# Kernel tuning notes

Measured on AMD Instinct MI355X. Metric: run time of the kernel, lower is better.

The kernel has to match this reference:

```python
import jax, jax.numpy as jnp
import numpy as np

B, C, H, W, K = 16, 512, 64, 64, 64  # K = external-attention latent dim (self.k = 64)


def setup_inputs() -> dict:
    key = jax.random.key(0)
    ks = jax.random.split(key, 5)
    x = jax.random.normal(ks[0], (B, C, H, W), dtype=jnp.float32)
    # conv1: Conv2d(c, c, 1) with bias; init normal(0, sqrt(2/(1*1*out_channels)))
    conv1_w = jax.random.normal(ks[1], (C, C), dtype=jnp.float32) * np.float32(np.sqrt(2.0 / C))
    conv1_b = jnp.zeros((C,), dtype=jnp.float32)
    # linear_0: Conv1d(c, k, 1, bias=False); init normal(0, sqrt(2/out_channels))
    lin0_w = jax.random.normal(ks[2], (K, C), dtype=jnp.float32) * np.float32(np.sqrt(2.0 / K))
    # linear_1: Conv1d(k, c, 1, bias=False)
    lin1_w = jax.random.normal(ks[3], (C, K), dtype=jnp.float32) * np.float32(np.sqrt(2.0 / C))
    # conv2: Conv2d(c, c, 1, bias=False)
    conv2_w = jax.random.normal(ks[4], (C, C), dtype=jnp.float32) * np.float32(np.sqrt(2.0 / C))
    return {"x": x, "conv1_w": conv1_w, "conv1_b": conv1_b,
            "lin0_w": lin0_w, "lin1_w": lin1_w, "conv2_w": conv2_w}


def reference(x, conv1_w, conv1_b, lin0_w, lin1_w, conv2_w):
    b, c, h, w = x.shape
    n = h * w
    idn = x
    # conv1: 1x1 conv == per-pixel GEMM
    y = jnp.einsum('oc,bchw->bohw', conv1_w, x) + conv1_b[None, :, None, None]
    y = y.reshape(b, c, n)
    # external attention: linear_0 -> softmax over tokens -> L1 renorm over latent dim
    attn = jnp.einsum('kc,bcn->bkn', lin0_w, y)          # (b, K, n)
    attn = jax.nn.softmax(attn, axis=-1)
    attn = attn / (1e-9 + attn.sum(axis=1, keepdims=True))
    y = jnp.einsum('ck,bkn->bcn', lin1_w, attn)          # (b, c, n)
    # rank: view(-1, c) row-major (as torch .view does), per-row topk threshold,
    # scale below-threshold by 0.75 and the rest by 1.25; output is detached
    # (torch.tensor(pred, requires_grad=False)) -> stop_gradient
    top_k = c // 2
    flat = y.reshape(-1, c)                               # (b*n, c) row-major chunks
    thr = jax.lax.top_k(flat, top_k)[0][:, -1:]           # k-th largest per row
    scaled = jnp.where(flat < thr, 0.75 * flat, 1.25 * flat)
    yr = jax.lax.stop_gradient(scaled).reshape(b, c, h, w)
    # conv2: 1x1 conv no bias + ReLU, residual add, final ReLU
    out = jax.nn.relu(jnp.einsum('oc,bchw->bohw', conv2_w, yr))
    return jax.nn.relu(out + idn)
```

## Files before the change

kernel.cpp:

```cpp
#include <hip/hip_runtime.h>
#include <stdint.h>

typedef unsigned short u16;
typedef unsigned int u32;
using short8 = __attribute__((ext_vector_type(8))) short;
using f32x4  = __attribute__((ext_vector_type(4))) float;

#define BDIM 16
#define CDIM 512
#define KLAT 64
#define NTOK 4096

__device__ __forceinline__ u16 f2bf(float x) {
  union { float f; u32 u; } a; a.f = x;
  u32 r = a.u + 0x7FFFu + ((a.u >> 16) & 1u);
  return (u16)(r >> 16);
}
__device__ __forceinline__ u32 pack2(float a, float b) {
  return (u32)f2bf(a) | ((u32)f2bf(b) << 16);
}

__global__ __launch_bounds__(256) void k_setup(
    const float* __restrict__ conv1_w, const float* __restrict__ conv1_b,
    const float* __restrict__ lin0_w,  const float* __restrict__ lin1_w,
    const float* __restrict__ conv2_w,
    u16* __restrict__ w0bf, float* __restrict__ b0,
    u16* __restrict__ lin1bf, u16* __restrict__ cwbf)
{
  const int bid = blockIdx.x;
  const int t = threadIdx.x;
  if (bid < 128) {
    const int kb = bid & 15, cb = bid >> 4;
    const int lane = t & 63;
    int k = kb * 4 + (t >> 6);
    k = __builtin_amdgcn_readfirstlane(k);
    const int c = cb * 64 + lane;
    float acc = 0.f;
    const float* l0 = lin0_w + (size_t)k * CDIM;
    const float* cw = conv1_w + c;
#pragma unroll 4
    for (int o = 0; o < CDIM; ++o)
      acc = fmaf(l0[o], cw[(size_t)o * CDIM], acc);
    w0bf[k * CDIM + c] = f2bf(acc);
  } else if (bid == 128) {
    if (t < KLAT) {
      float acc = 0.f;
      for (int c = 0; c < CDIM; ++c) acc = fmaf(lin0_w[t * CDIM + c], conv1_b[c], acc);
      b0[t] = acc;
    }
  } else if (bid < 193) {
    const int b2 = bid - 129;
    const float4* src = (const float4*)conv2_w;
#pragma unroll
    for (int i = 0; i < 4; ++i) {
      int idx = (b2 * 256 + t) + i * 16384;
      float4 v = src[idx];
      uint2 o;
      o.x = pack2(v.x, v.y);
      o.y = pack2(v.z, v.w);
      *(uint2*)(cwbf + (size_t)idx * 4) = o;
    }
  } else {
    const int b2 = bid - 193;
#pragma unroll
    for (int i = 0; i < 4; ++i) {
      int g = b2 * 1024 + i * 256 + t;
      float4 v0 = *(const float4*)(lin1_w + (size_t)g * 8);
      float4 v1 = *(const float4*)(lin1_w + (size_t)g * 8 + 4);
      uint4 o;
      o.x = pack2(v0.x, v0.y); o.y = pack2(v0.z, v0.w);
      o.z = pack2(v1.x, v1.y); o.w = pack2(v1.z, v1.w);
      *(uint4*)(lin1bf + (size_t)g * 8) = o;
    }
  }
}

__global__ __launch_bounds__(256) void k_xpose(
    const float* __restrict__ x, u16* __restrict__ xbt)
{
  __shared__ float tile[32 * 512];
  const int n0 = blockIdx.x * 512, c0 = blockIdx.y * 32, b = blockIdx.z;
  const int t = threadIdx.x;
#pragma unroll
  for (int i = 0; i < 16; ++i) {
    int f4 = t + i * 256;
    int row = f4 >> 7, col4 = f4 & 127;
    float4 v = *(const float4*)(x + ((size_t)(b * CDIM + c0 + row)) * NTOK + n0 + col4 * 4);
    int phys4 = (col4 + row + (row >> 3)) & 127;
    *(float4*)&tile[row * 512 + phys4 * 4] = v;
  }
  __syncthreads();
#pragma unroll
  for (int i = 0; i < 8; ++i) {
    int nr = (t >> 2) + i * 64;
    int cs = (t & 3) * 8;
    float w[8];
#pragma unroll
    for (int j = 0; j < 8; ++j) {
      int row = cs + j;
      int phys4 = ((nr >> 2) + row + (row >> 3)) & 127;
      w[j] = tile[row * 512 + phys4 * 4 + (nr & 3)];
    }
    uint4 o;
    o.x = pack2(w[0], w[1]); o.y = pack2(w[2], w[3]);
    o.z = pack2(w[4], w[5]); o.w = pack2(w[6], w[7]);
    *(uint4*)(xbt + ((size_t)(b * NTOK + n0 + nr)) * CDIM + c0 + cs) = o;
  }
}

__global__ __launch_bounds__(256) void k_logits(
    const u16* __restrict__ w0bf, const u16* __restrict__ xbt,
    const float* __restrict__ b0, float* __restrict__ logits)
{
  __shared__ u16 As[64 * 72];
  __shared__ u16 Bs[128 * 72];
  const int nb = blockIdx.x, b = blockIdx.y;
  const int t = threadIdx.x;
  const int wv = t >> 6, lane = t & 63;
  const int quad = lane >> 4, l15 = lane & 15;
  f32x4 acc[4][2];
#pragma unroll
  for (int mi = 0; mi < 4; ++mi)
#pragma unroll
    for (int ni = 0; ni < 2; ++ni) acc[mi][ni] = (f32x4){0.f, 0.f, 0.f, 0.f};

  for (int kc = 0; kc < 8; ++kc) {
#pragma unroll
    for (int i = 0; i < 2; ++i) {
      int ch = t + i * 256;
      int row = ch >> 3, col = (ch & 7) * 8;
      uint4 a = *(const uint4*)(w0bf + (size_t)row * CDIM + kc * 64 + col);
      *(uint4*)&As[row * 72 + col] = a;
    }
#pragma unroll
    for (int i = 0; i < 4; ++i) {
      int ch = t + i * 256;
      int row = ch >> 3, col = (ch & 7) * 8;
      uint4 bb = *(const uint4*)(xbt + ((size_t)(b * NTOK + nb * 128 + row)) * CDIM + kc * 64 + col);
      *(uint4*)&Bs[row * 72 + col] = bb;
    }
    __syncthreads();
#pragma unroll
    for (int kk = 0; kk < 2; ++kk) {
      short8 af[4], bf_[2];
#pragma unroll
      for (int mi = 0; mi < 4; ++mi)
        af[mi] = *(short8*)&As[(mi * 16 + l15) * 72 + kk * 32 + quad * 8];
#pragma unroll
      for (int ni = 0; ni < 2; ++ni)
        bf_[ni] = *(short8*)&Bs[(wv * 32 + ni * 16 + l15) * 72 + kk * 32 + quad * 8];
#pragma unroll
      for (int mi = 0; mi < 4; ++mi)
#pragma unroll
        for (int ni = 0; ni < 2; ++ni)
          acc[mi][ni] = __builtin_amdgcn_mfma_f32_16x16x32_bf16(
              af[mi], bf_[ni], acc[mi][ni], 0, 0, 0);
    }
    __syncthreads();
  }
#pragma unroll
  for (int mi = 0; mi < 4; ++mi) {
#pragma unroll
    for (int ni = 0; ni < 2; ++ni) {
#pragma unroll
      for (int r = 0; r < 4; ++r) {
        int row = mi * 16 + quad * 4 + r;
        int col = nb * 128 + wv * 32 + ni * 16 + l15;
        logits[((size_t)(b * KLAT + row)) * NTOK + col] = acc[mi][ni][r] + b0[row];
      }
    }
  }
}

__global__ __launch_bounds__(256) void k_softmax(float* __restrict__ attn)
{
  __shared__ float red[4], red2[4];
  const int t = threadIdx.x;
  float* p = attn + (size_t)blockIdx.x * NTOK;
  float4 v[4];
#pragma unroll
  for (int i = 0; i < 4; ++i) v[i] = ((float4*)p)[t + i * 256];
  float m = v[0].x;
#pragma unroll
  for (int i = 0; i < 4; ++i)
    m = fmaxf(m, fmaxf(fmaxf(v[i].x, v[i].y), fmaxf(v[i].z, v[i].w)));
#pragma unroll
  for (int o = 1; o < 64; o <<= 1) m = fmaxf(m, __shfl_xor(m, o));
  const int wv = t >> 6, lane = t & 63;
  if (lane == 0) red[wv] = m;
  __syncthreads();
  m = fmaxf(fmaxf(red[0], red[1]), fmaxf(red[2], red[3]));
  float s = 0.f;
#pragma unroll
  for (int i = 0; i < 4; ++i) {
    v[i].x = __expf(v[i].x - m); s += v[i].x;
    v[i].y = __expf(v[i].y - m); s += v[i].y;
    v[i].z = __expf(v[i].z - m); s += v[i].z;
    v[i].w = __expf(v[i].w - m); s += v[i].w;
  }
#pragma unroll
  for (int o = 1; o < 64; o <<= 1) s += __shfl_xor(s, o);
  if (lane == 0) red2[wv] = s;
  __syncthreads();
  s = red2[0] + red2[1] + red2[2] + red2[3];
  const float inv = 1.f / s;
#pragma unroll
  for (int i = 0; i < 4; ++i) {
    v[i].x *= inv; v[i].y *= inv; v[i].z *= inv; v[i].w *= inv;
    ((float4*)p)[t + i * 256] = v[i];
  }
}

__global__ __launch_bounds__(256) void k_attnT(
    const float* __restrict__ attn, u16* __restrict__ attnT)
{
  __shared__ float tile[64 * 256];
  __shared__ float inv_[256];
  const int n0 = blockIdx.x * 256, b = blockIdx.y;
  const int t = threadIdx.x;
#pragma unroll
  for (int i = 0; i < 16; ++i) {
    int f4 = t + i * 256;
    int row = f4 >> 6, col4 = f4 & 63;
    float4 v = *(const float4*)(attn + ((size_t)(b * KLAT + row)) * NTOK + n0 + col4 * 4);
    int phys4 = (col4 + row + (row >> 3)) & 63;
    *(float4*)&tile[row * 256 + phys4 * 4] = v;
  }
  __syncthreads();
  {
    int n4 = t >> 2, sub = t & 3;
    float s = 0.f;
#pragma unroll
    for (int k = 0; k < 64; ++k) {
      int phys4 = (n4 + k + (k >> 3)) & 63;
      s += tile[k * 256 + phys4 * 4 + sub];
    }
    inv_[t] = 1.f / (1e-9f + s);
  }
  __syncthreads();
#pragma unroll
  for (int i = 0; i < 8; ++i) {
    int nr = (t >> 3) + i * 32;
    int cs = (t & 7) * 8;
    float sc = inv_[nr];
    float w[8];
#pragma unroll
    for (int j = 0; j < 8; ++j) {
      int row = cs + j;
      int phys4 = ((nr >> 2) + row + (row >> 3)) & 63;
      w[j] = tile[row * 256 + phys4 * 4 + (nr & 3)] * sc;
    }
    uint4 o;
    o.x = pack2(w[0], w[1]); o.y = pack2(w[2], w[3]);
    o.z = pack2(w[4], w[5]); o.w = pack2(w[6], w[7]);
    *(uint4*)(attnT + ((size_t)(b * NTOK + n0 + nr)) * KLAT + cs) = o;
  }
}

__global__ __launch_bounds__(256) void k_lin1mm(
    const u16* __restrict__ lin1bf, const u16* __restrict__ attnT,
    float* __restrict__ y2)
{
  __shared__ u16 As[128 * 72];
  __shared__ u16 Bs[128 * 72];
  const int nb = blockIdx.x, mb = blockIdx.y, b = blockIdx.z;
  const int t = threadIdx.x;
  const int wv = t >> 6, lane = t & 63;
  const int wm = wv >> 1, wn = wv & 1;
  const int quad = lane >> 4, l15 = lane & 15;
  f32x4 acc[4][4];
#pragma unroll
  for (int mi = 0; mi < 4; ++mi)
#pragma unroll
    for (int ni = 0; ni < 4; ++ni) acc[mi][ni] = (f32x4){0.f, 0.f, 0.f, 0.f};

#pragma unroll
  for (int i = 0; i < 4; ++i) {
    int ch = t + i * 256;
    int row = ch >> 3, col = (ch & 7) * 8;
    uint4 a = *(const uint4*)(lin1bf + ((size_t)(mb * 128 + row)) * KLAT + col);
    *(uint4*)&As[row * 72 + col] = a;
    uint4 bb = *(const uint4*)(attnT + ((size_t)(b * NTOK + nb * 128 + row)) * KLAT + col);
    *(uint4*)&Bs[row * 72 + col] = bb;
  }
  __syncthreads();
#pragma unroll
  for (int kk = 0; kk < 2; ++kk) {
    short8 af[4], bf_[4];
#pragma unroll
    for (int mi = 0; mi < 4; ++mi)
      af[mi] = *(short8*)&As[(wm * 64 + mi * 16 + l15) * 72 + kk * 32 + quad * 8];
#pragma unroll
    for (int ni = 0; ni < 4; ++ni)
      bf_[ni] = *(short8*)&Bs[(wn * 64 + ni * 16 + l15) * 72 + kk * 32 + quad * 8];
#pragma unroll
    for (int mi = 0; mi < 4; ++mi)
#pragma unroll
      for (int ni = 0; ni < 4; ++ni)
        acc[mi][ni] = __builtin_amdgcn_mfma_f32_16x16x32_bf16(
            af[mi], bf_[ni], acc[mi][ni], 0, 0, 0);
  }
#pragma unroll
  for (int mi = 0; mi < 4; ++mi) {
#pragma unroll
    for (int ni = 0; ni < 4; ++ni) {
#pragma unroll
      for (int r = 0; r < 4; ++r) {
        int row = mb * 128 + wm * 64 + mi * 16 + quad * 4 + r;
        int col = nb * 128 + wn * 64 + ni * 16 + l15;
        y2[((size_t)(b * CDIM + row)) * NTOK + col] = acc[mi][ni][r];
      }
    }
  }
}

__global__ __launch_bounds__(256) void k_rank(
    const float* __restrict__ y2, u16* __restrict__ yrt)
{
  __shared__ float tile[32 * 512];
  const int n0 = blockIdx.x * 512, c0 = blockIdx.y * 32, b = blockIdx.z;
  const int t = threadIdx.x;
#pragma unroll
  for (int i = 0; i < 16; ++i) {
    int f4 = t + i * 256;
    int row = f4 >> 7, col4 = f4 & 127;
    float4 v = *(const float4*)(y2 + ((size_t)(b * CDIM + c0 + row)) * NTOK + n0 + col4 * 4);
    int phys4 = (col4 + row + (row >> 3)) & 127;
    *(float4*)&tile[row * 512 + phys4 * 4] = v;
  }
  __syncthreads();
  const int wv = t >> 6, lane = t & 63;
  for (int r = 0; r < 8; ++r) {
    const int row = wv * 8 + r;
    const int rot = row + (row >> 3);
    const int c4a = (lane + rot) & 127;
    const int c4b = (64 + lane + rot) & 127;
    float* pa = &tile[row * 512 + c4a * 4];
    float* pb = &tile[row * 512 + c4b * 4];
    float4 va = *(const float4*)pa;
    float4 vb = *(const float4*)pb;
    float v[8] = {va.x, va.y, va.z, va.w, vb.x, vb.y, vb.z, vb.w};
    u32 key[8];
#pragma unroll
    for (int j = 0; j < 8; ++j) {
      u32 u = __float_as_uint(v[j]);
      key[j] = (u & 0x80000000u) ? ~u : (u | 0x80000000u);
    }
    u32 lo = 0u, hi = 0xFFFFFFFFu;
    u32 thr;
    for (;;) {
      u32 d = hi - lo;
      u32 mid = lo + (d >> 1) + (d & 1u);
      int cnt = 0;
#pragma unroll
      for (int j = 0; j < 8; ++j)
        cnt += (int)__popcll(__ballot(key[j] >= mid));
      if (cnt == 256) { thr = mid; break; }
      if (cnt > 256) lo = mid; else hi = mid - 1u;
      if (lo >= hi) { thr = lo; break; }
    }
    float4 oa, ob;
    oa.x = (key[0] < thr) ? 0.75f * v[0] : 1.25f * v[0];
    oa.y = (key[1] < thr) ? 0.75f * v[1] : 1.25f * v[1];
    oa.z = (key[2] < thr) ? 0.75f * v[2] : 1.25f * v[2];
    oa.w = (key[3] < thr) ? 0.75f * v[3] : 1.25f * v[3];
    ob.x = (key[4] < thr) ? 0.75f * v[4] : 1.25f * v[4];
    ob.y = (key[5] < thr) ? 0.75f * v[5] : 1.25f * v[5];
    ob.z = (key[6] < thr) ? 0.75f * v[6] : 1.25f * v[6];
    ob.w = (key[7] < thr) ? 0.75f * v[7] : 1.25f * v[7];
    *(float4*)pa = oa;
    *(float4*)pb = ob;
  }
  __syncthreads();
#pragma unroll
  for (int i = 0; i < 8; ++i) {
    int nr = (t >> 2) + i * 64;
    int cs = (t & 3) * 8;
    float w[8];
#pragma unroll
    for (int j = 0; j < 8; ++j) {
      int row = cs + j;
      int phys4 = ((nr >> 2) + row + (row >> 3)) & 127;
      w[j] = tile[row * 512 + phys4 * 4 + (nr & 3)];
    }
    uint4 o;
    o.x = pack2(w[0], w[1]); o.y = pack2(w[2], w[3]);
    o.z = pack2(w[4], w[5]); o.w = pack2(w[6], w[7]);
    *(uint4*)(yrt + ((size_t)(b * NTOK + n0 + nr)) * CDIM + c0 + cs) = o;
  }
}

__global__ __launch_bounds__(256) void k_conv2(
    const u16* __restrict__ cwbf, const u16* __restrict__ yrt,
    const float* __restrict__ x, float* __restrict__ out)
{
  __shared__ u16 As[128 * 72];
  __shared__ u16 Bs[128 * 72];
  const int nb = blockIdx.x, mb = blockIdx.y, b = blockIdx.z;
  const int t = threadIdx.x;
  const int wv = t >> 6, lane = t & 63;
  const int wm = wv >> 1, wn = wv & 1;
  const int quad = lane >> 4, l15 = lane & 15;
  f32x4 acc[4][4];
#pragma unroll
  for (int mi = 0; mi < 4; ++mi)
#pragma unroll
    for (int ni = 0; ni < 4; ++ni) acc[mi][ni] = (f32x4){0.f, 0.f, 0.f, 0.f};

  for (int kc = 0; kc < 8; ++kc) {
#pragma unroll
    for (int i = 0; i < 4; ++i) {
      int ch = t + i * 256;
      int row = ch >> 3, col = (ch & 7) * 8;
      uint4 a = *(const uint4*)(cwbf + ((size_t)(mb * 128 + row)) * CDIM + kc * 64 + col);
      *(uint4*)&As[row * 72 + col] = a;
      uint4 bb = *(const uint4*)(yrt + ((size_t)(b * NTOK + nb * 128 + row)) * CDIM + kc * 64 + col);
      *(uint4*)&Bs[row * 72 + col] = bb;
    }
    __syncthreads();
#pragma unroll
    for (int kk = 0; kk < 2; ++kk) {
      short8 af[4], bf_[4];
#pragma unroll
      for (int mi = 0; mi < 4; ++mi)
        af[mi] = *(short8*)&As[(wm * 64 + mi * 16 + l15) * 72 + kk * 32 + quad * 8];
#pragma unroll
      for (int ni = 0; ni < 4; ++ni)
        bf_[ni] = *(short8*)&Bs[(wn * 64 + ni * 16 + l15) * 72 + kk * 32 + quad * 8];
#pragma unroll
      for (int mi = 0; mi < 4; ++mi)
#pragma unroll
        for (int ni = 0; ni < 4; ++ni)
          acc[mi][ni] = __builtin_amdgcn_mfma_f32_16x16x32_bf16(
              af[mi], bf_[ni], acc[mi][ni], 0, 0, 0);
    }
    __syncthreads();
  }
#pragma unroll
  for (int mi = 0; mi < 4; ++mi) {
#pragma unroll
    for (int ni = 0; ni < 4; ++ni) {
#pragma unroll
      for (int r = 0; r < 4; ++r) {
        int row = mb * 128 + wm * 64 + mi * 16 + quad * 4 + r;
        int col = nb * 128 + wn * 64 + ni * 16 + l15;
        size_t off = ((size_t)(b * CDIM + row)) * NTOK + col;
        float g = fmaxf(acc[mi][ni][r], 0.f) + x[off];
        out[off] = fmaxf(g, 0.f);
      }
    }
  }
}

extern "C" void kernel_launch(void* const* d_in, const int* in_sizes, int n_in,
                              void* d_out, int out_size, void* d_ws, size_t ws_size,
                              hipStream_t stream)
{
  const float* x       = (const float*)d_in[0];
  const float* conv1_w = (const float*)d_in[1];
  const float* conv1_b = (const float*)d_in[2];
  const float* lin0_w  = (const float*)d_in[3];
  const float* lin1_w  = (const float*)d_in[4];
  const float* conv2_w = (const float*)d_in[5];
  float* out = (float*)d_out;

  char* ws = (char*)d_ws;
  float* attn  = (float*)ws;
  u16*   xbt   = (u16*)(ws + 16777216);
  u16*   attnT = xbt;
  u16*   yrt   = xbt;
  char*  wsm   = ws + 16777216 + 67108864;
  u16*   w0bf  = (u16*)wsm;
  float* b0    = (float*)(wsm + 131072);
  u16*   lin1bf= (u16*)(wsm + 131328);
  u16*   cwbf  = (u16*)(wsm + 262400);
  float* y2    = out;

  k_setup  <<<197, 256, 0, stream>>>(conv1_w, conv1_b, lin0_w, lin1_w, conv2_w,
                                     w0bf, b0, lin1bf, cwbf);
  k_xpose  <<<dim3(8, 16, 16), 256, 0, stream>>>(x, xbt);
  k_logits <<<dim3(32, 16), 256, 0, stream>>>(w0bf, xbt, b0, attn);
  k_softmax<<<1024, 256, 0, stream>>>(attn);
  k_attnT  <<<dim3(16, 16), 256, 0, stream>>>(attn, attnT);
  k_lin1mm <<<dim3(32, 4, 16), 256, 0, stream>>>(lin1bf, attnT, y2);
  k_rank   <<<dim3(8, 16, 16), 256, 0, stream>>>(y2, yrt);
  k_conv2  <<<dim3(32, 4, 16), 256, 0, stream>>>(cwbf, yrt, x, out);
}
```

Before: 526.5 us.

## Fuse lin1 GEMM into rank kernel and batch radix threshold search

Merges the lin1 matmul with the top-k rank kernel, so each block computes its 32x512 tile of y with MFMA directly into shared memory. This removes the 128 MB fp32 y2 round trip through global memory. The per-row binary search is replaced by a fixed 32-step bitwise radix selection over 8 rows at a time, which removes divergent early exits and adds ILP. attnT now lives in the output buffer so it does not alias yrt, at the cost of recomputing the tiny lin1 GEMM loads per block and higher register use.

```diff
diff --git a/kernel.cpp b/kernel.cpp
--- a/kernel.cpp
+++ b/kernel.cpp
@@ -18,6 +18,15 @@
 }
 __device__ __forceinline__ u32 pack2(float a, float b) {
   return (u32)f2bf(a) | ((u32)f2bf(b) << 16);
+}
+__device__ __forceinline__ u32 f2key(float x) {
+  u32 u = __float_as_uint(x);
+  return (u & 0x80000000u) ? ~u : (u | 0x80000000u);
+}
+__device__ __forceinline__ float keyscale(u32 k_, u32 thr) {
+  u32 u = (k_ & 0x80000000u) ? (k_ & 0x7FFFFFFFu) : ~k_;
+  float v = __uint_as_float(u);
+  return (k_ < thr) ? 0.75f * v : 1.25f * v;
 }
 
 __global__ __launch_bounds__(256) void k_setup(
@@ -257,121 +266,100 @@
   }
 }
 
-__global__ __launch_bounds__(256) void k_lin1mm(
+__global__ __launch_bounds__(256) void k_lin1rank(
     const u16* __restrict__ lin1bf, const u16* __restrict__ attnT,
-    float* __restrict__ y2)
-{
-  __shared__ u16 As[128 * 72];
-  __shared__ u16 Bs[128 * 72];
-  const int nb = blockIdx.x, mb = blockIdx.y, b = blockIdx.z;
-  const int t = threadIdx.x;
-  const int wv = t >> 6, lane = t & 63;
-  const int wm = wv >> 1, wn = wv & 1;
-  const int quad = lane >> 4, l15 = lane & 15;
-  f32x4 acc[4][4];
-#pragma unroll
-  for (int mi = 0; mi < 4; ++mi)
-#pragma unroll
-    for (int ni = 0; ni < 4; ++ni) acc[mi][ni] = (f32x4){0.f, 0.f, 0.f, 0.f};
-
-#pragma unroll
-  for (int i = 0; i < 4; ++i) {
-    int ch = t + i * 256;
-    int row = ch >> 3, col = (ch & 7) * 8;
-    uint4 a = *(const uint4*)(lin1bf + ((size_t)(mb * 128 + row)) * KLAT + col);
-    *(uint4*)&As[row * 72 + col] = a;
-    uint4 bb = *(const uint4*)(attnT + ((size_t)(b * NTOK + nb * 128 + row)) * KLAT + col);
-    *(uint4*)&Bs[row * 72 + col] = bb;
-  }
-  __syncthreads();
-#pragma unroll
-  for (int kk = 0; kk < 2; ++kk) {
-    short8 af[4], bf_[4];
-#pragma unroll
-    for (int mi = 0; mi < 4; ++mi)
-      af[mi] = *(short8*)&As[(wm * 64 + mi * 16 + l15) * 72 + kk * 32 + quad * 8];
-#pragma unroll
-    for (int ni = 0; ni < 4; ++ni)
-      bf_[ni] = *(short8*)&Bs[(wn * 64 + ni * 16 + l15) * 72 + kk * 32 + quad * 8];
-#pragma unroll
-    for (int mi = 0; mi < 4; ++mi)
-#pragma unroll
-      for (int ni = 0; ni < 4; ++ni)
-        acc[mi][ni] = __builtin_amdgcn_mfma_f32_16x16x32_bf16(
-            af[mi], bf_[ni], acc[mi][ni], 0, 0, 0);
-  }
-#pragma unroll
-  for (int mi = 0; mi < 4; ++mi) {
-#pragma unroll
-    for (int ni = 0; ni < 4; ++ni) {
-#pragma unroll
-      for (int r = 0; r < 4; ++r) {
-        int row = mb * 128 + wm * 64 + mi * 16 + quad * 4 + r;
-        int col = nb * 128 + wn * 64 + ni * 16 + l15;
-        y2[((size_t)(b * CDIM + row)) * NTOK + col] = acc[mi][ni][r];
-      }
-    }
-  }
-}
-
-__global__ __launch_bounds__(256) void k_rank(
-    const float* __restrict__ y2, u16* __restrict__ yrt)
+    u16* __restrict__ yrt)
 {
   __shared__ float tile[32 * 512];
   const int n0 = blockIdx.x * 512, c0 = blockIdx.y * 32, b = blockIdx.z;
   const int t = threadIdx.x;
-#pragma unroll
-  for (int i = 0; i < 16; ++i) {
-    int f4 = t + i * 256;
-    int row = f4 >> 7, col4 = f4 & 127;
-    float4 v = *(const float4*)(y2 + ((size_t)(b * CDIM + c0 + row)) * NTOK + n0 + col4 * 4);
-    int phys4 = (col4 + row + (row >> 3)) & 127;
-    *(float4*)&tile[row * 512 + phys4 * 4] = v;
-  }
-  __syncthreads();
   const int wv = t >> 6, lane = t & 63;
+  const int quad = lane >> 4, l15 = lane & 15;
+
+  short8 af[2][2], bfr[8][2];
+#pragma unroll
+  for (int mi = 0; mi < 2; ++mi)
+#pragma unroll
+    for (int kk = 0; kk < 2; ++kk)
+      af[mi][kk] = *(const short8*)(lin1bf +
+          (size_t)(c0 + mi * 16 + l15) * KLAT + kk * 32 + quad * 8);
+#pragma unroll
+  for (int ni = 0; ni < 8; ++ni)
+#pragma unroll
+    for (int kk = 0; kk < 2; ++kk)
+      bfr[ni][kk] = *(const short8*)(attnT +
+          ((size_t)(b * NTOK + n0 + wv * 128 + ni * 16 + l15)) * KLAT + kk * 32 + quad * 8);
+  f32x4 acc[2][8];
+#pragma unroll
+  for (int mi = 0; mi < 2; ++mi)
+#pragma unroll
+    for (int ni = 0; ni < 8; ++ni) acc[mi][ni] = (f32x4){0.f, 0.f, 0.f, 0.f};
+#pragma unroll
+  for (int kk = 0; kk < 2; ++kk)
+#pragma unroll
+    for (int mi = 0; mi < 2; ++mi)
+#pragma unroll
+      for (int ni = 0; ni < 8; ++ni)
+        acc[mi][ni] = __builtin_amdgcn_mfma_f32_16x16x32_bf16(
+            af[mi][kk], bfr[ni][kk], acc[mi][ni], 0, 0, 0);
+#pragma unroll
+  for (int mi = 0; mi < 2; ++mi) {
+#pragma unroll
+    for (int ni = 0; ni < 8; ++ni) {
+#pragma unroll
+      for (int r = 0; r < 4; ++r) {
+        int row = mi * 16 + quad * 4 + r;
+        int col = wv * 128 + ni * 16 + l15;
+        int phys4 = ((col >> 2) + row + (row >> 3)) & 127;
+        tile[row * 512 + phys4 * 4 + (col & 3)] = acc[mi][ni][r];
+      }
+    }
+  }
+  __syncthreads();
+
+  u32 key[8][8];
+#pragma unroll
   for (int r = 0; r < 8; ++r) {
     const int row = wv * 8 + r;
     const int rot = row + (row >> 3);
     const int c4a = (lane + rot) & 127;
     const int c4b = (64 + lane + rot) & 127;
-    float* pa = &tile[row * 512 + c4a * 4];
-    float* pb = &tile[row * 512 + c4b * 4];
-    float4 va = *(const float4*)pa;
-    float4 vb = *(const float4*)pb;
-    float v[8] = {va.x, va.y, va.z, va.w, vb.x, vb.y, vb.z, vb.w};
-    u32 key[8];
-#pragma unroll
-    for (int j = 0; j < 8; ++j) {
-      u32 u = __float_as_uint(v[j]);
-      key[j] = (u & 0x80000000u) ? ~u : (u | 0x80000000u);
-    }
-    u32 lo = 0u, hi = 0xFFFFFFFFu;
-    u32 thr;
-    for (;;) {
-      u32 d = hi - lo;
-      u32 mid = lo + (d >> 1) + (d & 1u);
+    float4 va = *(const float4*)&tile[row * 512 + c4a * 4];
+    float4 vb = *(const float4*)&tile[row * 512 + c4b * 4];
+    key[r][0] = f2key(va.x); key[r][1] = f2key(va.y);
+    key[r][2] = f2key(va.z); key[r][3] = f2key(va.w);
+    key[r][4] = f2key(vb.x); key[r][5] = f2key(vb.y);
+    key[r][6] = f2key(vb.z); key[r][7] = f2key(vb.w);
+  }
+  u32 thr[8] = {0u, 0u, 0u, 0u, 0u, 0u, 0u, 0u};
+  for (int bit = 31; bit >= 0; --bit) {
+    const u32 m = 1u << bit;
+#pragma unroll
+    for (int r = 0; r < 8; ++r) {
+      u32 cand = thr[r] | m;
       int cnt = 0;
 #pragma unroll
       for (int j = 0; j < 8; ++j)
-        cnt += (int)__popcll(__ballot(key[j] >= mid));
-      if (cnt == 256) { thr = mid; break; }
-      if (cnt > 256) lo = mid; else hi = mid - 1u;
-      if (lo >= hi) { thr = lo; break; }
-    }
+        cnt += (int)__popcll(__ballot(key[r][j] >= cand));
+      if (cnt >= 256) thr[r] = cand;
+    }
+  }
+#pragma unroll
+  for (int r = 0; r < 8; ++r) {
+    const int row = wv * 8 + r;
+    const int rot = row + (row >> 3);
+    const int c4a = (lane + rot) & 127;
+    const int c4b = (64 + lane + rot) & 127;
     float4 oa, ob;
-    oa.x = (key[0] < thr) ? 0.75f * v[0] : 1.25f * v[0];
-    oa.y = (key[1] < thr) ? 0.75f * v[1] : 1.25f * v[1];
-    oa.z = (key[2] < thr) ? 0.75f * v[2] : 1.25f * v[2];
-    oa.w = (key[3] < thr) ? 0.75f * v[3] : 1.25f * v[3];
-    ob.x = (key[4] < thr) ? 0.75f * v[4] : 1.25f * v[4];
-    ob.y = (key[5] < thr) ? 0.75f * v[5] : 1.25f * v[5];
-    ob.z = (key[6] < thr) ? 0.75f * v[6] : 1.25f * v[6];
-    ob.w = (key[7] < thr) ? 0.75f * v[7] : 1.25f * v[7];
-    *(float4*)pa = oa;
-    *(float4*)pb = ob;
-  }
-  __syncthreads();
+    oa.x = keyscale(key[r][0], thr[r]); oa.y = keyscale(key[r][1], thr[r]);
+    oa.z = keyscale(key[r][2], thr[r]); oa.w = keyscale(key[r][3], thr[r]);
+    ob.x = keyscale(key[r][4], thr[r]); ob.y = keyscale(key[r][5], thr[r]);
+    ob.z = keyscale(key[r][6], thr[r]); ob.w = keyscale(key[r][7], thr[r]);
+    *(float4*)&tile[row * 512 + c4a * 4] = oa;
+    *(float4*)&tile[row * 512 + c4b * 4] = ob;
+  }
+  __syncthreads();
+
 #pragma unroll
   for (int i = 0; i < 8; ++i) {
     int nr = (t >> 2) + i * 64;
@@ -467,22 +455,20 @@
   char* ws = (char*)d_ws;
   float* attn  = (float*)ws;
   u16*   xbt   = (u16*)(ws + 16777216);
-  u16*   attnT = xbt;
   u16*   yrt   = xbt;
+  u16*   attnT = (u16*)d_out;
   char*  wsm   = ws + 16777216 + 67108864;
   u16*   w0bf  = (u16*)wsm;
   float* b0    = (float*)(wsm + 131072);
   u16*   lin1bf= (u16*)(wsm + 131328);
   u16*   cwbf  = (u16*)(wsm + 262400);
-  float* y2    = out;
-
-  k_setup  <<<197, 256, 0, stream>>>(conv1_w, conv1_b, lin0_w, lin1_w, conv2_w,
-                                     w0bf, b0, lin1bf, cwbf);
-  k_xpose  <<<dim3(8, 16, 16), 256, 0, stream>>>(x, xbt);
-  k_logits <<<dim3(32, 16), 256, 0, stream>>>(w0bf, xbt, b0, attn);
-  k_softmax<<<1024, 256, 0, stream>>>(attn);
-  k_attnT  <<<dim3(16, 16), 256, 0, stream>>>(attn, attnT);
-  k_lin1mm <<<dim3(32, 4, 16), 256, 0, stream>>>(lin1bf, attnT, y2);
-  k_rank   <<<dim3(8, 16, 16), 256, 0, stream>>>(y2, yrt);
-  k_conv2  <<<dim3(32, 4, 16), 256, 0, stream>>>(cwbf, yrt, x, out);
-}
+
+  k_setup   <<<197, 256, 0, stream>>>(conv1_w, conv1_b, lin0_w, lin1_w, conv2_w,
+                                      w0bf, b0, lin1bf, cwbf);
+  k_xpose   <<<dim3(8, 16, 16), 256, 0, stream>>>(x, xbt);
+  k_logits  <<<dim3(32, 16), 256, 0, stream>>>(w0bf, xbt, b0, attn);
+  k_softmax <<<1024, 256, 0, stream>>>(attn);
+  k_attnT   <<<dim3(16, 16), 256, 0, stream>>>(attn, attnT);
+  k_lin1rank<<<dim3(8, 16, 16), 256, 0, stream>>>(lin1bf, attnT, yrt);
+  k_conv2   <<<dim3(32, 4, 16), 256, 0, stream>>>(cwbf, yrt, x, out);
+}
```

Result: no change. 535.9 us (+1.8%).
